# Kernel tuning notes

Measured on AMD Instinct MI355X. Metric: run time of the kernel, lower is better.

Reference implementation:

```python
import jax, jax.numpy as jnp
import numpy as np

B, C, H, W = 2, 256, 64, 64
NH = 4          # num_heads -> ch = C // NH = 64
G = 32          # GroupNorm groups (normalization(channels))
EPS = 1e-5


def setup_inputs() -> dict:
    key = jax.random.key(0)
    ks = jax.random.split(key, 7)
    s = 1.0 / np.sqrt(C).astype(np.float32)
    return {
        "x": jax.random.normal(ks[0], (B, C, H, W), jnp.float32),
        "gn_scale": 1.0 + 0.02 * jax.random.normal(ks[1], (C,), jnp.float32),
        "gn_bias": 0.02 * jax.random.normal(ks[2], (C,), jnp.float32),
        "w_qkv": s * jax.random.normal(ks[3], (3 * C, C), jnp.float32),
        "b_qkv": jnp.zeros((3 * C,), jnp.float32),
        # NOTE: original zero-inits proj_out; we use random weights so the
        # attention path contributes to the output (meaningful baseline).
        "w_proj": s * jax.random.normal(ks[4], (C, C), jnp.float32),
        "b_proj": jnp.zeros((C,), jnp.float32),
    }


def reference(x, gn_scale, gn_bias, w_qkv, b_qkv, w_proj, b_proj):
    b, c = x.shape[0], x.shape[1]
    spatial = x.shape[2:]
    t = int(np.prod(spatial))
    xf = x.reshape(b, c, t)                      # [B, C, T]

    # GroupNorm(32) over (channels-in-group, T)
    xg = xf.reshape(b, G, c // G, t)
    mu = xg.mean(axis=(2, 3), keepdims=True)
    var = xg.var(axis=(2, 3), keepdims=True)
    xn = ((xg - mu) * jax.lax.rsqrt(var + EPS)).reshape(b, c, t)
    xn = xn * gn_scale[None, :, None] + gn_bias[None, :, None]

    # 1x1 conv -> qkv: [B, 3C, T]
    qkv = jnp.einsum('oc,bct->bot', w_qkv, xn) + b_qkv[None, :, None]

    # QKVAttentionLegacy: reshape (B*H, 3*ch, T) then split
    ch = c // NH
    qkv_h = qkv.reshape(b * NH, 3 * ch, t)
    q, k, v = jnp.split(qkv_h, 3, axis=1)        # each [B*H, ch, T]
    scale = 1.0 / np.sqrt(np.sqrt(ch)).astype(np.float32)
    w = jnp.einsum('bct,bcs->bts', q * scale, k * scale)   # [B*H, T, T]
    w = jax.nn.softmax(w.astype(jnp.float32), axis=-1).astype(qkv.dtype)
    a = jnp.einsum('bts,bcs->bct', w, v).reshape(b, c, t)  # [B, C, T]

    # proj 1x1 conv + residual
    h = jnp.einsum('oc,bct->bot', w_proj, a) + b_proj[None, :, None]
    return (xf + h).reshape(b, c, *spatial)
```

## Files before the change

### kernel.cpp

```cpp
#include <hip/hip_runtime.h>
#include <math.h>

#define T 4096
#define C 256
#define BATCH 2
#define NH 4
#define G 32
#define CPG 8
#define EPS 1e-5f
#define LOG2E 1.4426950408889634f
#define QSCALE (0.125f * LOG2E)
#define KSPLIT 4
#define KRANGE (T / KSPLIT)
#define KTILE 128
#define NIT (KRANGE / KTILE)
#define BH (BATCH * NH)

typedef __attribute__((ext_vector_type(8))) short bfv8;
typedef __attribute__((ext_vector_type(4))) short bfv4;
typedef __attribute__((ext_vector_type(4))) float f32x4;
typedef __attribute__((ext_vector_type(2))) float f32x2;
typedef __attribute__((ext_vector_type(16))) float f32x16;

static __device__ __forceinline__ short f2bf(float f) {
    union { float f; unsigned u; } v; v.f = f;
    return (short)((v.u + 0x7FFFu + ((v.u >> 16) & 1u)) >> 16);
}
static __device__ __forceinline__ float bf2f(short s) {
    union { float f; unsigned u; } v; v.u = ((unsigned)(unsigned short)s) << 16;
    return v.f;
}

#if __has_builtin(__builtin_amdgcn_exp2f)
#define EXP2(x) __builtin_amdgcn_exp2f(x)
#else
#define EXP2(x) exp2f(x)
#endif

#define AS1 __attribute__((address_space(1)))
#define AS3 __attribute__((address_space(3)))
static __device__ __forceinline__ void gll16(const void* g, void* l) {
    __builtin_amdgcn_global_load_lds((const AS1 void*)g, (AS3 void*)l, 16, 0, 0);
}

__global__ __launch_bounds__(256) void prep_stats(
    const float* __restrict__ wq, const float* __restrict__ wp,
    short* __restrict__ wqb, short* __restrict__ wpb,
    const float* __restrict__ x, float* __restrict__ gnp)
{
    __shared__ float rs[256], rss[256];
    const int bid = blockIdx.x;
    const int tid = threadIdx.x;
    if (bid < 256) {
        int i = bid * 256 + tid;
        const int NQ = 768 * 256 / 4;
        float4 v; short* dst;
        if (i < NQ) { v = ((const float4*)wq)[i]; dst = wqb + i * 4; }
        else        { int j = i - NQ; v = ((const float4*)wp)[j]; dst = wpb + j * 4; }
        bfv4 o = { f2bf(v.x), f2bf(v.y), f2bf(v.z), f2bf(v.w) };
        *(bfv4*)dst = o;
        return;
    }
    const int blk = (bid - 256) >> 2;
    const int ts  = (bid - 256) & 3;
    const int b = blk / G, g = blk % G;
    const float* xp = x + ((size_t)b * C + g * CPG) * T + ts * 1024;

    float s = 0.f, ss = 0.f;
    #pragma unroll
    for (int u = 0; u < CPG; u++) {
        float4 v = ((const float4*)(xp + (size_t)u * T))[tid];
        s  += v.x + v.y + v.z + v.w;
        ss += v.x*v.x + v.y*v.y + v.z*v.z + v.w*v.w;
    }
    rs[tid] = s; rss[tid] = ss;
    __syncthreads();
    for (int off = 128; off > 0; off >>= 1) {
        if (tid < off) { rs[tid] += rs[tid+off]; rss[tid] += rss[tid+off]; }
        __syncthreads();
    }
    if (tid == 0) {
        gnp[(blk * 4 + ts) * 2 + 0] = rs[0];
        gnp[(blk * 4 + ts) * 2 + 1] = rss[0];
    }
}

__global__ __launch_bounds__(256) void gn_norm(const float* __restrict__ x,
                                               const float* __restrict__ scale,
                                               const float* __restrict__ bias,
                                               const float* __restrict__ gnp,
                                               short* __restrict__ xnT) {
    const int blk = blockIdx.x;
    const int ts  = blockIdx.y;
    const int b = blk / G, g = blk % G;
    const int c0 = g * CPG;
    const float* xp = x + ((size_t)b * C + c0) * T;

    float s = 0.f, ss = 0.f;
    #pragma unroll
    for (int i = 0; i < 4; i++) {
        s  += gnp[(blk * 4 + i) * 2 + 0];
        ss += gnp[(blk * 4 + i) * 2 + 1];
    }
    const float inv_n = 1.0f / (CPG * T);
    const float mu  = s * inv_n;
    const float var = ss * inv_n - mu * mu;
    const float rstd = rsqrtf(var + EPS);

    float sc[CPG], bi[CPG];
    #pragma unroll
    for (int u = 0; u < CPG; u++) {
        sc[u] = scale[c0+u] * rstd;
        bi[u] = bias[c0+u] - mu * sc[u];
    }

    const int t = ts * 1024 + threadIdx.x * 4;
    float vv[CPG][4];
    #pragma unroll
    for (int u = 0; u < CPG; u++) {
        float4 v = *(const float4*)&xp[(size_t)u * T + t];
        vv[u][0] = v.x * sc[u] + bi[u];
        vv[u][1] = v.y * sc[u] + bi[u];
        vv[u][2] = v.z * sc[u] + bi[u];
        vv[u][3] = v.w * sc[u] + bi[u];
    }
    #pragma unroll
    for (int j = 0; j < 4; j++) {
        bfv8 w = { f2bf(vv[0][j]), f2bf(vv[1][j]), f2bf(vv[2][j]), f2bf(vv[3][j]),
                   f2bf(vv[4][j]), f2bf(vv[5][j]), f2bf(vv[6][j]), f2bf(vv[7][j]) };
        *(bfv8*)&xnT[((size_t)b * T + t + j) * C + c0] = w;
    }
}

__global__ __launch_bounds__(256) void gemm_qkv(
    const short* __restrict__ wq,
    const float* __restrict__ bq,
    const short* __restrict__ xnT,
    short* __restrict__ qb, short* __restrict__ kb, short* __restrict__ vb)
{
    const int b  = blockIdx.z;
    const int t0 = blockIdx.x * 64;
    const int ot = blockIdx.y;
    const int h = ot / 3, part = ot % 3;
    const int o0 = ot * 64;

    __shared__ short sm[8192];
    short* Ab = sm;
    short* Bb = sm + 4096;

    const int tid = threadIdx.x, lane = tid & 63, wave = tid >> 6;
    const int col = lane & 15, quad = lane >> 4;
    const short* xb = xnT + (size_t)b * T * C;

    f32x4 acc[4];
    #pragma unroll
    for (int g = 0; g < 4; g++) { acc[g][0]=0.f; acc[g][1]=0.f; acc[g][2]=0.f; acc[g][3]=0.f; }

    for (int k0 = 0; k0 < C; k0 += 64) {
        __syncthreads();
        #pragma unroll
        for (int hh = 0; hh < 2; hh++) {
            gll16(wq + (size_t)(o0 + 16*wave + col) * C + k0 + hh*32 + quad*8,
                  Ab + (hh*4 + wave) * 512);
            gll16(xb + (size_t)(t0 + 16*wave + col) * C + k0 + hh*32 + quad*8,
                  Bb + (hh*4 + wave) * 512);
        }
        __syncthreads();
        #pragma unroll
        for (int hh = 0; hh < 2; hh++) {
            bfv8 af = *(const bfv8*)(Ab + (hh*4 + wave) * 512 + lane*8);
            #pragma unroll
            for (int g = 0; g < 4; g++) {
                bfv8 bf = *(const bfv8*)(Bb + (hh*4 + g) * 512 + lane*8);
                acc[g] = __builtin_amdgcn_mfma_f32_16x16x32_bf16(af, bf, acc[g], 0, 0, 0);
            }
        }
    }

    const int olocal = 16*wave + quad*4;
    float bias_r[4];
    #pragma unroll
    for (int r = 0; r < 4; r++) bias_r[r] = bq[o0 + olocal + r];
    const size_t hd = (size_t)(b * NH + h);

    if (part < 2) {
        short* dst = (part == 0 ? qb : kb) + hd * T * 64;
        const float sc = (part == 0) ? QSCALE : 1.0f;
        #pragma unroll
        for (int g = 0; g < 4; g++) {
            int t = t0 + 16*g + col;
            bfv4 w = { f2bf((acc[g][0] + bias_r[0]) * sc),
                       f2bf((acc[g][1] + bias_r[1]) * sc),
                       f2bf((acc[g][2] + bias_r[2]) * sc),
                       f2bf((acc[g][3] + bias_r[3]) * sc) };
            *(bfv4*)&dst[(size_t)t * 64 + olocal] = w;
        }
    } else {
        short* dst = vb + hd * 64 * T;
        #pragma unroll
        for (int g = 0; g < 4; g++)
            #pragma unroll
            for (int r = 0; r < 4; r++)
                dst[(size_t)(olocal + r) * T + t0 + 16*g + col] =
                    f2bf(acc[g][r] + bias_r[r]);
    }
}

__global__ __launch_bounds__(512, 4) void attn_kernel(
    const short* __restrict__ qb,
    const short* __restrict__ kb,
    const short* __restrict__ vb,
    short* __restrict__ opart,
    float* __restrict__ lp)
{
    __shared__ short smem[32768];
    const int flat = blockIdx.x;
    const int bh = flat & 7;
    const int tb = (flat >> 3) & 15;
    const int ks = flat >> 7;
    const int t0 = tb * 256;
    const int k0base = ks * KRANGE;
    const short* kbh = kb + (size_t)bh * T * 64;
    const short* vbh = vb + (size_t)bh * 64 * T;

    const int tid  = threadIdx.x;
    const int lane = tid & 63;
    const int wave = tid >> 6;
    const int klow = lane & 31;
    const int hi   = lane >> 5;
    const int swz  = klow & 7;
    const int vswz = klow & 15;

    const int q = t0 + wave*32 + klow;
    const short* qrow = qb + (size_t)bh * T * 64 + (size_t)q * 64;
    bfv8 qf[4];
    #pragma unroll
    for (int s = 0; s < 4; s++) qf[s] = *(const bfv8*)(qrow + s*16 + hi*8);

    f32x16 oacc[2];
    #pragma unroll
    for (int c = 0; c < 2; c++)
        #pragma unroll
        for (int r = 0; r < 16; r++) oacc[c][r] = 0.f;
    f32x2 l2 = { 0.f, 0.f };

    const int lr8  = lane >> 3, lc8  = lane & 7;
    const int lr16 = lane >> 4, lc16 = lane & 15;
    #define STAGE_KV(buf, s0)                                                   \
        {                                                                       \
            short* base = smem + (buf) * 16384;                                 \
            const int r0 = (wave*2+0)*8 + lr8;                                  \
            const int r1 = (wave*2+1)*8 + lr8;                                  \
            gll16(kbh + (size_t)((s0) + r0) * 64 + ((lc8 ^ (r0&7))<<3),         \
                  base + (wave*2+0)*512);                                       \
            gll16(kbh + (size_t)((s0) + r1) * 64 + ((lc8 ^ (r1&7))<<3),         \
                  base + (wave*2+1)*512);                                       \
            const int v0r = (wave*2+0)*4 + lr16;                                \
            const int v1r = (wave*2+1)*4 + lr16;                                \
            gll16(vbh + (size_t)v0r * T + (s0) + ((lc16 ^ (v0r&15))<<3),        \
                  base + 8192 + (wave*2+0)*512);                                \
            gll16(vbh + (size_t)v1r * T + (s0) + ((lc16 ^ (v1r&15))<<3),        \
                  base + 8192 + (wave*2+1)*512);                                \
        }

    STAGE_KV(0, k0base)

    for (int it = 0; it < NIT; it++) {
        __syncthreads();
        if (it + 1 < NIT) STAGE_KV((it+1) & 1, k0base + (it+1)*KTILE)

        const short* kvb = smem + (it & 1) * 16384;
        const short* kl = kvb + klow*64;
        const short* vl = kvb + 8192 + klow*128 + 4*hi;

        #pragma unroll
        for (int kt = 0; kt < 4; kt++) {
            f32x16 sacc;
            #pragma unroll
            for (int r = 0; r < 16; r++) sacc[r] = 0.f;
            #pragma unroll
            for (int s = 0; s < 4; s++) {
                bfv8 kf = *(const bfv8*)(kl + kt*2048 + (((2*s+hi) ^ swz) << 3));
                sacc = __builtin_amdgcn_mfma_f32_32x32x16_bf16(kf, qf[s], sacc, 0, 0, 0);
            }
            #pragma unroll
            for (int u = 0; u < 2; u++) {
                float p[8];
                #pragma unroll
                for (int j = 0; j < 8; j++) p[j] = EXP2(sacc[8*u + j]);
                f32x2 pa = { p[0], p[1] }, pb = { p[2], p[3] };
                f32x2 pc = { p[4], p[5] }, pd = { p[6], p[7] };
                l2 += (pa + pb) + (pc + pd);
                union { unsigned w[4]; bfv8 v; } pk_;
                #pragma unroll
                for (int w = 0; w < 4; w++)
                    asm("v_cvt_pk_bf16_f32 %0, %1, %2"
                        : "=v"(pk_.w[w]) : "v"(p[2*w]), "v"(p[2*w+1]));
                const int kc = 2*kt + u;
                #pragma unroll
                for (int c = 0; c < 2; c++) {
                    bfv4 v0 = *(const bfv4*)(vl + c*4096 + (((2*kc)   ^ vswz) << 3));
                    bfv4 v1 = *(const bfv4*)(vl + c*4096 + (((2*kc+1) ^ vswz) << 3));
                    bfv8 vf = { v0[0], v0[1], v0[2], v0[3],
                                v1[0], v1[1], v1[2], v1[3] };
                    oacc[c] = __builtin_amdgcn_mfma_f32_32x32x16_bf16(
                                  vf, pk_.v, oacc[c], 0, 0, 0);
                }
            }
        }
    }

    float lsum = l2[0] + l2[1];
    lsum += __shfl_xor(lsum, 32);

    const size_t rowbase = (size_t)(ks*BH + bh) * T + t0 + wave*32;
    short* opb = opart + (rowbase + klow) * 64;
    #pragma unroll
    for (int c = 0; c < 2; c++)
        #pragma unroll
        for (int u = 0; u < 4; u++) {
            bfv4 w = { f2bf(oacc[c][4*u+0]), f2bf(oacc[c][4*u+1]),
                       f2bf(oacc[c][4*u+2]), f2bf(oacc[c][4*u+3]) };
            *(bfv4*)(opb + c*32 + u*8 + hi*4) = w;
        }
    if (hi == 0) {
        lp[rowbase + klow] = lsum;
    }
}

__global__ __launch_bounds__(256) void gemm_proj(
    const short* __restrict__ wp,
    const float* __restrict__ bp,
    const short* __restrict__ opart,
    const float* __restrict__ lp,
    const float* __restrict__ x,
    float* __restrict__ out)
{
    const int b  = blockIdx.z;
    const int t0 = blockIdx.x * 64;
    const int o0 = blockIdx.y * 64;

    __shared__ short sm[8192];
    short* Ab = sm;
    short* Bb = sm + 4096;

    const int tid = threadIdx.x, lane = tid & 63, wave = tid >> 6;
    const int col = lane & 15, quad = lane >> 4;

    const int trow = t0 + 16*wave + col;
    float rl4[NH];
    #pragma unroll
    for (int hh = 0; hh < NH; hh++) {
        float ls = 0.f;
        #pragma unroll
        for (int ks = 0; ks < KSPLIT; ks++)
            ls += lp[((size_t)(ks*BH) + b*NH + hh) * T + trow];
        rl4[hh] = 1.0f / ls;
    }

    f32x4 acc[4];
    #pragma unroll
    for (int g = 0; g < 4; g++) { acc[g][0]=0.f; acc[g][1]=0.f; acc[g][2]=0.f; acc[g][3]=0.f; }

    for (int k0 = 0; k0 < C; k0 += 64) {
        __syncthreads();
        #pragma unroll
        for (int hh = 0; hh < 2; hh++) {
            gll16(wp + (size_t)(o0 + 16*wave + col) * C + k0 + hh*32 + quad*8,
                  Ab + (hh*4 + wave) * 512);
            const int chg = k0 + hh*32 + quad*8;
            const int hd = chg >> 6, chin = chg & 63;
            const short* ob = opart + (((size_t)(b*NH + hd)) * T + trow) * 64 + chin;
            float a8[8] = {0.f,0.f,0.f,0.f,0.f,0.f,0.f,0.f};
            #pragma unroll
            for (int ks = 0; ks < KSPLIT; ks++) {
                bfv8 v = *(const bfv8*)(ob + (size_t)ks * BH * T * 64);
                #pragma unroll
                for (int u = 0; u < 8; u++) a8[u] += bf2f(v[u]);
            }
            const float rl = rl4[hd];
            bfv8 pk;
            #pragma unroll
            for (int u = 0; u < 8; u++) pk[u] = f2bf(a8[u] * rl);
            *(bfv8*)(Bb + (hh*4 + wave) * 512 + lane*8) = pk;
        }
        __syncthreads();
        #pragma unroll
        for (int hh = 0; hh < 2; hh++) {
            bfv8 af = *(const bfv8*)(Ab + (hh*4 + wave) * 512 + lane*8);
            #pragma unroll
            for (int g = 0; g < 4; g++) {
                bfv8 bf = *(const bfv8*)(Bb + (hh*4 + g) * 512 + lane*8);
                acc[g] = __builtin_amdgcn_mfma_f32_16x16x32_bf16(af, bf, acc[g], 0, 0, 0);
            }
        }
    }

    const int olocal = 16*wave + quad*4;
    #pragma unroll
    for (int r = 0; r < 4; r++) {
        const int o = o0 + olocal + r;
        const float bias = bp[o];
        const size_t rowoff = ((size_t)b * C + o) * T;
        #pragma unroll
        for (int g = 0; g < 4; g++) {
            const size_t idx = rowoff + t0 + 16*g + col;
            out[idx] = acc[g][r] + bias + x[idx];
        }
    }
}

extern "C" void kernel_launch(void* const* d_in, const int* in_sizes, int n_in,
                              void* d_out, int out_size, void* d_ws, size_t ws_size,
                              hipStream_t stream) {
    (void)in_sizes; (void)n_in; (void)out_size; (void)ws_size;
    const float* x        = (const float*)d_in[0];
    const float* gn_scale = (const float*)d_in[1];
    const float* gn_bias  = (const float*)d_in[2];
    const float* w_qkv    = (const float*)d_in[3];
    const float* b_qkv    = (const float*)d_in[4];
    const float* w_proj   = (const float*)d_in[5];
    const float* b_proj   = (const float*)d_in[6];
    float* out = (float*)d_out;

    short* ws    = (short*)d_ws;
    short* qb    = ws;
    short* kb    = qb  + (size_t)BH * T * 64;
    short* vb    = kb  + (size_t)BH * T * 64;
    short* xnT   = vb  + (size_t)BH * T * 64;
    short* wqb   = xnT + (size_t)BATCH * T * C;
    short* wpb   = wqb + 768 * 256;
    short* opart = wpb + 256 * 256;
    float* lp    = (float*)(opart + (size_t)KSPLIT * BH * T * 64);
    float* gnp   = lp + (size_t)KSPLIT * BH * T;

    prep_stats<<<dim3(512), 256, 0, stream>>>(w_qkv, w_proj, wqb, wpb, x, gnp);
    gn_norm<<<dim3(BATCH * G, 4), 256, 0, stream>>>(x, gn_scale, gn_bias, gnp, xnT);
    gemm_qkv<<<dim3(T/64, 12, BATCH), 256, 0, stream>>>(wqb, b_qkv, xnT, qb, kb, vb);
    attn_kernel<<<dim3(512), 512, 0, stream>>>(qb, kb, vb, opart, lp);
    gemm_proj<<<dim3(T/64, 4, BATCH), 256, 0, stream>>>(wpb, b_proj, opart, lp, x, out);
}
```

Before: 149.4 us.

## Store K/V in LDS in MFMA fragment order and permute V columns

The V projection output now writes columns in a permuted order so each lane's eight bf16 values are contiguous. The attention kernel's global-to-LDS staging places K and V tiles in fragment-major order. Each lane then reads its K or V operand with one linear 16-byte LDS load instead of XOR-swizzled addresses and two 8-byte loads stitched together. This trades bank-conflict-avoiding swizzles for conflict-free linear reads and cuts LDS instruction count, but it depends on the permutation matching the MFMA operand layout.

Measured after the change: 146.8 us (median of 2 runs). No clear change (-1.7%).

```diff
diff --git a/kernel.cpp b/kernel.cpp
--- a/kernel.cpp
+++ b/kernel.cpp
@@ -197,11 +197,12 @@
         }
     } else {
         short* dst = vb + hd * 64 * T;
+        const int pcol = (col & 3) | ((col & 4) << 1) | ((col & 8) >> 1);
         #pragma unroll
         for (int g = 0; g < 4; g++)
             #pragma unroll
             for (int r = 0; r < 4; r++)
-                dst[(size_t)(olocal + r) * T + t0 + 16*g + col] =
+                dst[(size_t)(olocal + r) * T + t0 + 16*g + pcol] =
                     f2bf(acc[g][r] + bias_r[r]);
     }
 }
@@ -228,8 +229,6 @@
     const int wave = tid >> 6;
     const int klow = lane & 31;
     const int hi   = lane >> 5;
-    const int swz  = klow & 7;
-    const int vswz = klow & 15;
 
     const int q = t0 + wave*32 + klow;
     const short* qrow = qb + (size_t)bh * T * 64 + (size_t)q * 64;
@@ -244,23 +243,20 @@
         for (int r = 0; r < 16; r++) oacc[c][r] = 0.f;
     f32x2 l2 = { 0.f, 0.f };
 
-    const int lr8  = lane >> 3, lc8  = lane & 7;
-    const int lr16 = lane >> 4, lc16 = lane & 15;
+    const int n1 = tid, n2 = tid + 512;
+    const int kOff1 = ((n1>>8)*32 + (n1&31))*64 + ((n1>>6)&3)*16 + ((n1>>5)&1)*8;
+    const int kOff2 = ((n2>>8)*32 + (n2&31))*64 + ((n2>>6)&3)*16 + ((n2>>5)&1)*8;
+    const size_t vRow1 = (size_t)(((n1>>9)<<5) + (n1&31)) * T;
+    const size_t vRow2 = (size_t)(((n2>>9)<<5) + (n2&31)) * T;
+    const int vCol1 = ((n1>>6)&7)*16 + ((n1>>5)&1)*8;
+    const int vCol2 = ((n2>>6)&7)*16 + ((n2>>5)&1)*8;
     #define STAGE_KV(buf, s0)                                                   \
         {                                                                       \
             short* base = smem + (buf) * 16384;                                 \
-            const int r0 = (wave*2+0)*8 + lr8;                                  \
-            const int r1 = (wave*2+1)*8 + lr8;                                  \
-            gll16(kbh + (size_t)((s0) + r0) * 64 + ((lc8 ^ (r0&7))<<3),         \
-                  base + (wave*2+0)*512);                                       \
-            gll16(kbh + (size_t)((s0) + r1) * 64 + ((lc8 ^ (r1&7))<<3),         \
-                  base + (wave*2+1)*512);                                       \
-            const int v0r = (wave*2+0)*4 + lr16;                                \
-            const int v1r = (wave*2+1)*4 + lr16;                                \
-            gll16(vbh + (size_t)v0r * T + (s0) + ((lc16 ^ (v0r&15))<<3),        \
-                  base + 8192 + (wave*2+0)*512);                                \
-            gll16(vbh + (size_t)v1r * T + (s0) + ((lc16 ^ (v1r&15))<<3),        \
-                  base + 8192 + (wave*2+1)*512);                                \
+            gll16(kbh + (size_t)(s0) * 64 + kOff1, base + n1*8);                \
+            gll16(kbh + (size_t)(s0) * 64 + kOff2, base + n2*8);                \
+            gll16(vbh + vRow1 + (s0) + vCol1, base + 8192 + n1*8);              \
+            gll16(vbh + vRow2 + (s0) + vCol2, base + 8192 + n2*8);              \
         }
 
     STAGE_KV(0, k0base)
@@ -270,8 +266,6 @@
         if (it + 1 < NIT) STAGE_KV((it+1) & 1, k0base + (it+1)*KTILE)
 
         const short* kvb = smem + (it & 1) * 16384;
-        const short* kl = kvb + klow*64;
-        const short* vl = kvb + 8192 + klow*128 + 4*hi;
 
         #pragma unroll
         for (int kt = 0; kt < 4; kt++) {
@@ -280,7 +274,7 @@
             for (int r = 0; r < 16; r++) sacc[r] = 0.f;
             #pragma unroll
             for (int s = 0; s < 4; s++) {
-                bfv8 kf = *(const bfv8*)(kl + kt*2048 + (((2*s+hi) ^ swz) << 3));
+                bfv8 kf = *(const bfv8*)(kvb + ((kt*4 + s)*64 + lane)*8);
                 sacc = __builtin_amdgcn_mfma_f32_32x32x16_bf16(kf, qf[s], sacc, 0, 0, 0);
             }
             #pragma unroll
@@ -299,10 +293,7 @@
                 const int kc = 2*kt + u;
                 #pragma unroll
                 for (int c = 0; c < 2; c++) {
-                    bfv4 v0 = *(const bfv4*)(vl + c*4096 + (((2*kc)   ^ vswz) << 3));
-                    bfv4 v1 = *(const bfv4*)(vl + c*4096 + (((2*kc+1) ^ vswz) << 3));
-                    bfv8 vf = { v0[0], v0[1], v0[2], v0[3],
-                                v1[0], v1[1], v1[2], v1[3] };
+                    bfv8 vf = *(const bfv8*)(kvb + 8192 + ((c*8 + kc)*64 + lane)*8);
                     oacc[c] = __builtin_amdgcn_mfma_f32_32x32x16_bf16(
                                   vf, pk_.v, oacc[c], 0, 0, 0);
                 }
```
